# Kernel tuning notes

Measured on AMD Instinct MI355X. Metric: run time of the kernel, lower is better.

## Reference

```python
import jax, jax.numpy as jnp
import numpy as np
from jax import lax

VOCAB = 100   # chars_count
E = 32        # CHARACTER_EMBEDDING_SIZE
H = 64        # CHAR_LSTM_HIDDEN_SIZE
N_WORDS = 65536
MAX_LEN = 16


def setup_inputs() -> dict:
    key = jax.random.key(0)
    k_ch, k_len, k_emb, k_wih, k_whh, k_bih, k_bhh = jax.random.split(key, 7)
    chars = jax.random.randint(k_ch, (N_WORDS, MAX_LEN), 0, VOCAB, dtype=jnp.int32)
    lengths = jax.random.randint(k_len, (N_WORDS,), 1, MAX_LEN + 1, dtype=jnp.int32)
    s = 1.0 / np.sqrt(H)  # torch LSTM default init scale
    emb = jax.random.normal(k_emb, (VOCAB, E), dtype=jnp.float32)
    W_ih = jax.random.uniform(k_wih, (4 * H, E), minval=-s, maxval=s, dtype=jnp.float32)
    W_hh = jax.random.uniform(k_whh, (4 * H, H), minval=-s, maxval=s, dtype=jnp.float32)
    b_ih = jax.random.uniform(k_bih, (4 * H,), minval=-s, maxval=s, dtype=jnp.float32)
    b_hh = jax.random.uniform(k_bhh, (4 * H,), minval=-s, maxval=s, dtype=jnp.float32)
    return {"emb": emb, "W_ih": W_ih, "W_hh": W_hh, "b_ih": b_ih, "b_hh": b_hh,
            "chars": chars, "lengths": lengths}


def _char_lstm(emb, W_ih, W_hh, b_ih, b_hh, chars, lengths):
    N, L = chars.shape
    h0 = jnp.zeros((N, H), dtype=emb.dtype)
    c0 = jnp.zeros((N, H), dtype=emb.dtype)

    def step(carry, inp):
        h, c = carry
        ch_t, t = inp  # ch_t: [N] char ids at timestep t
        x = emb[ch_t]  # [N, E]
        gates = x @ W_ih.T + b_ih + h @ W_hh.T + b_hh  # [N, 4H]
        i_g, f_g, g_g, o_g = jnp.split(gates, 4, axis=-1)  # torch order i,f,g,o
        i_g = jax.nn.sigmoid(i_g)
        f_g = jax.nn.sigmoid(f_g)
        g_g = jnp.tanh(g_g)
        o_g = jax.nn.sigmoid(o_g)
        c_new = f_g * c + i_g * g_g
        h_new = o_g * jnp.tanh(c_new)
        active = (t < lengths)[:, None]  # freeze state past word end -> out[-1]
        h = jnp.where(active, h_new, h)
        c = jnp.where(active, c_new, c)
        return (h, c), None

    (h_final, _), _ = lax.scan(step, (h0, c0), (chars.T, jnp.arange(L)))
    return h_final  # [N, H] = last valid hidden per word


def reference(emb, W_ih, W_hh, b_ih, b_hh, chars, lengths):
    return _char_lstm(emb, W_ih, W_hh, b_ih, b_hh, chars, lengths)
```

## Files before the change

kernel.cpp:

```cpp
#include <hip/hip_runtime.h>
#include <hip/hip_bf16.h>


#define VOCAB 100
#define E     32
#define NW    65536
#define MAXL  16
#define NGRP  4096

typedef __bf16 bf16x8 __attribute__((ext_vector_type(8)));
typedef float  f32x4  __attribute__((ext_vector_type(4)));
typedef unsigned short ushort_t;
typedef unsigned int uint_t;

#define LOG2E    1.4426950408889634f
#define TWOLOG2E 2.8853900817779268f

__device__ __forceinline__ ushort_t f2bf(float x) {
    union { __hip_bfloat16 b; ushort_t u; } cv;
    cv.b = __float2bfloat16(x);
    return cv.u;
}
__device__ __forceinline__ float exp2_hw(float x) { return __builtin_amdgcn_exp2f(x); }
__device__ __forceinline__ float rcp_hw(float x)  { return __builtin_amdgcn_rcpf(x); }

__global__ void prep_fused(const float* __restrict__ emb, const float* __restrict__ Wih,
                           const float* __restrict__ Whh, const float* __restrict__ bih,
                           const float* __restrict__ bhh, const int* __restrict__ lengths,
                           float* __restrict__ xtab, ushort_t* __restrict__ Wb,
                           int* __restrict__ bh) {
    int bid = blockIdx.x;
    if (bid < VOCAB) {
        int ch = bid, g = threadIdx.x, q = g >> 6;
        float scl = (q == 2) ? TWOLOG2E : -LOG2E;
        float acc = bih[g] + bhh[g];
        const float* er = emb + ch * E;
        const float* wr = Wih + g * E;
        #pragma unroll
        for (int e = 0; e < E; ++e) acc = fmaf(er[e], wr[e], acc);
        xtab[ch * 256 + g] = acc * scl;
    } else if (bid < VOCAB + 64) {
        int i = (bid - VOCAB) * 256 + threadIdx.x;
        int q = i >> 12;
        float scl = (q == 2) ? TWOLOG2E : -LOG2E;
        Wb[i] = f2bf(Whh[i] * scl);
    } else {
        int blk = bid - (VOCAB + 64);
        __shared__ int h[16];
        if (threadIdx.x < 16) h[threadIdx.x] = 0;
        __syncthreads();
        atomicAdd(&h[lengths[blk * 256 + threadIdx.x] - 1], 1);
        __syncthreads();
        if (threadIdx.x < 16) bh[blk * 16 + threadIdx.x] = h[threadIdx.x];
    }
}

__global__ void k_bases(const int* __restrict__ bh, int* __restrict__ bases) {
    __shared__ int chunk[16][16], chunkpre[16][16], tot[16], gb[16];
    int t = threadIdx.x, b = t & 15, cs = t >> 4;
    int s = 0;
    #pragma unroll
    for (int i = 0; i < 16; ++i) s += bh[(cs * 16 + i) * 16 + b];
    chunk[cs][b] = s;
    __syncthreads();
    if (t < 16) {
        int a = 0;
        for (int c2 = 0; c2 < 16; ++c2) { chunkpre[c2][b] = a; a += chunk[c2][b]; }
        tot[b] = a;
    }
    __syncthreads();
    if (t == 0) { int a = 0; for (int i = 0; i < 16; ++i) { gb[i] = a; a += tot[i]; } }
    __syncthreads();
    int base = gb[b] + chunkpre[cs][b];
    for (int i = 0; i < 16; ++i) {
        bases[(cs * 16 + i) * 16 + b] = base;
        base += bh[(cs * 16 + i) * 16 + b];
    }
}

__global__ void k_scatter(const int* __restrict__ lengths, const int* __restrict__ bases,
                          int* __restrict__ perm) {
    __shared__ int h[16];
    if (threadIdx.x < 16) h[threadIdx.x] = 0;
    __syncthreads();
    int w = blockIdx.x * 256 + threadIdx.x;
    int b = lengths[w] - 1;
    int r = atomicAdd(&h[b], 1);
    perm[bases[blockIdx.x * 16 + b] + r] = w;
}

__global__ __launch_bounds__(256, 2) void lstm_main(
    const ushort_t* __restrict__ Wb, const float* __restrict__ xtab,
    const int* __restrict__ chars, const int* __restrict__ lengths,
    const int* __restrict__ perm, float* __restrict__ out)
{
    __shared__ __align__(16) char Hlds_all[4][2048];
    char* Hbase = Hlds_all[threadIdx.x >> 6];

    const int lane = threadIdx.x & 63;
    const int w  = lane & 15;
    const int lq = lane >> 4;
    const int widx = threadIdx.x >> 6;
    const int cls  = (widx << 2) | (blockIdx.x & 3);
    const int grp  = (cls << 8) | (blockIdx.x >> 2);

    bf16x8 a[16][2];
    #pragma unroll
    for (int m = 0; m < 16; ++m)
        #pragma unroll
        for (int kh = 0; kh < 2; ++kh)
            a[m][kh] = *reinterpret_cast<const bf16x8*>(Wb + ((m * 16 + w) * 64 + kh * 32 + lq * 8));

    const int sw = (w & 7) << 4;
    const int base_w = w * 128;
    int wr_off[4], rd_off[2];
    #pragma unroll
    for (int b = 0; b < 4; ++b) wr_off[b] = base_w + ((b * 32 + lq * 8) ^ sw);
    #pragma unroll
    for (int kh = 0; kh < 2; ++kh) rd_off[kh] = base_w + ((kh * 64 + lq * 16) ^ sw);

    const int wid = perm[grp * 16 + w];
    const int len = lengths[wid];
    int ml = len;
    ml = max(ml, __shfl_xor(ml, 1));
    ml = max(ml, __shfl_xor(ml, 2));
    ml = max(ml, __shfl_xor(ml, 4));
    ml = max(ml, __shfl_xor(ml, 8));
    const int maxl = __builtin_amdgcn_readfirstlane(ml);
    const int* chp = chars + wid * MAXL;

    float hreg[4][4], creg[4][4];
    #pragma unroll
    for (int b = 0; b < 4; ++b)
        #pragma unroll
        for (int r = 0; r < 4; ++r) { hreg[b][r] = 0.f; creg[b][r] = 0.f; }

    int ch = chp[0];
    const float* xrow = xtab + ch * 256;
    f32x4 xtb[2][4];
    #pragma unroll
    for (int q = 0; q < 4; ++q)
        xtb[0][q] = *reinterpret_cast<const f32x4*>(xrow + (q * 4 + 0) * 16 + lq * 4);

    #pragma unroll 1
    for (int t = 0; t < maxl; ++t) {
        const int tn = (t + 1 < maxl) ? t + 1 : t;
        const int ch_nxt = chp[tn];
        const float* xrow_n = xtab + ch_nxt * 256;

        bf16x8 B0, B1;
        if (t > 0) {
            asm volatile("s_waitcnt lgkmcnt(0)" ::: "memory");
            B0 = *reinterpret_cast<const bf16x8*>(Hbase + rd_off[0]);
            B1 = *reinterpret_cast<const bf16x8*>(Hbase + rd_off[1]);
        }
        const bool act = (t < len);

        #pragma unroll
        for (int b = 0; b < 4; ++b) {
            if (b < 3) {
                #pragma unroll
                for (int q = 0; q < 4; ++q)
                    xtb[(b + 1) & 1][q] = *reinterpret_cast<const f32x4*>(xrow + (q * 4 + b + 1) * 16 + lq * 4);
            } else {
                #pragma unroll
                for (int q = 0; q < 4; ++q)
                    xtb[0][q] = *reinterpret_cast<const f32x4*>(xrow_n + q * 64 + lq * 4);
            }
            f32x4 d[4];
            #pragma unroll
            for (int q = 0; q < 4; ++q) d[q] = xtb[b & 1][q];
            if (t > 0) {
                #pragma unroll
                for (int q = 0; q < 4; ++q) {
                    d[q] = __builtin_amdgcn_mfma_f32_16x16x32_bf16(a[q * 4 + b][0], B0, d[q], 0, 0, 0);
                    d[q] = __builtin_amdgcn_mfma_f32_16x16x32_bf16(a[q * 4 + b][1], B1, d[q], 0, 0, 0);
                }
            }
            #pragma unroll
            for (int r = 0; r < 4; ++r) {
                float ig = rcp_hw(1.f + exp2_hw(d[0][r]));
                float fg = rcp_hw(1.f + exp2_hw(d[1][r]));
                float gg = fmaf(-2.f, rcp_hw(1.f + exp2_hw(d[2][r])), 1.f);
                float og = rcp_hw(1.f + exp2_hw(d[3][r]));
                float cn = fmaf(fg, creg[b][r], ig * gg);
                float tc = fmaf(-2.f, rcp_hw(1.f + exp2_hw(cn * TWOLOG2E)), 1.f);
                float hn = og * tc;
                creg[b][r] = act ? cn : creg[b][r];
                hreg[b][r] = act ? hn : hreg[b][r];
            }
            uint_t lo = (uint_t)f2bf(hreg[b][0]) | ((uint_t)f2bf(hreg[b][1]) << 16);
            uint_t hi = (uint_t)f2bf(hreg[b][2]) | ((uint_t)f2bf(hreg[b][3]) << 16);
            *reinterpret_cast<uint2*>(Hbase + wr_off[b]) = make_uint2(lo, hi);
        }
        ch = ch_nxt;
        xrow = xrow_n;
    }

    #pragma unroll
    for (int b = 0; b < 4; ++b) {
        f32x4 o;
        #pragma unroll
        for (int r = 0; r < 4; ++r) o[r] = hreg[b][r];
        *reinterpret_cast<f32x4*>(out + wid * 64 + b * 16 + lq * 4) = o;
    }
}

extern "C" void kernel_launch(void* const* d_in, const int* in_sizes, int n_in,
                              void* d_out, int out_size, void* d_ws, size_t ws_size,
                              hipStream_t stream) {
    const float* emb = (const float*)d_in[0];
    const float* Wih = (const float*)d_in[1];
    const float* Whh = (const float*)d_in[2];
    const float* bih = (const float*)d_in[3];
    const float* bhh = (const float*)d_in[4];
    const int* chars = (const int*)d_in[5];
    const int* lens  = (const int*)d_in[6];
    float* out = (float*)d_out;

    float*    xtab = (float*)d_ws;
    ushort_t* Wb   = (ushort_t*)(xtab + 25600);
    int*      bh   = (int*)(Wb + 16384);
    int*      bas  = bh + 4096;
    int*      perm = bas + 4096;

    prep_fused<<<VOCAB + 64 + 256, 256, 0, stream>>>(emb, Wih, Whh, bih, bhh, lens, xtab, Wb, bh);
    k_bases<<<1, 256, 0, stream>>>(bh, bas);
    k_scatter<<<256, 256, 0, stream>>>(lens, bas, perm);

    lstm_main<<<1024, 256, 0, stream>>>(Wb, xtab, chars, lens, perm, out);
}
```

Measured before the change: 177.8 us.

## Merge sort kernels, pair long and short groups per wave, share rcp in gates

Merges the bases and scatter kernels into a single k_sort kernel, where each block recomputes its own prefix from the shared histogram, removing one launch. The LSTM kernel now launches 512 blocks, and each wave processes two length-sorted groups: group i and group NGRP-1-i. This pairs short words with long ones to balance work across waves and reuses the weight fragments loaded into registers. The gate math folds sigmoid(i)*tanh(g) and sigmoid(o)*tanh(c) into a single reciprocal each, cutting rcp instructions at some risk of overflow in the products for extreme inputs. Each wave now runs its two groups one after the other, so fewer waves are resident to hide latency.

```diff
diff --git a/kernel.cpp b/kernel.cpp
--- a/kernel.cpp
+++ b/kernel.cpp
@@ -24,11 +24,11 @@
 __device__ __forceinline__ float exp2_hw(float x) { return __builtin_amdgcn_exp2f(x); }
 __device__ __forceinline__ float rcp_hw(float x)  { return __builtin_amdgcn_rcpf(x); }
 
-__global__ void prep_fused(const float* __restrict__ emb, const float* __restrict__ Wih,
-                           const float* __restrict__ Whh, const float* __restrict__ bih,
-                           const float* __restrict__ bhh, const int* __restrict__ lengths,
-                           float* __restrict__ xtab, ushort_t* __restrict__ Wb,
-                           int* __restrict__ bh) {
+__global__ void prep_all(const float* __restrict__ emb, const float* __restrict__ Wih,
+                         const float* __restrict__ Whh, const float* __restrict__ bih,
+                         const float* __restrict__ bhh, const int* __restrict__ lengths,
+                         float* __restrict__ xtab, ushort_t* __restrict__ Wb,
+                         int* __restrict__ bh) {
     int bid = blockIdx.x;
     if (bid < VOCAB) {
         int ch = bid, g = threadIdx.x, q = g >> 6;
@@ -55,38 +55,30 @@
     }
 }
 
-__global__ void k_bases(const int* __restrict__ bh, int* __restrict__ bases) {
-    __shared__ int chunk[16][16], chunkpre[16][16], tot[16], gb[16];
-    int t = threadIdx.x, b = t & 15, cs = t >> 4;
-    int s = 0;
-    #pragma unroll
-    for (int i = 0; i < 16; ++i) s += bh[(cs * 16 + i) * 16 + b];
-    chunk[cs][b] = s;
+__global__ void k_sort(const int* __restrict__ lengths, const int* __restrict__ bh,
+                       int* __restrict__ perm) {
+    __shared__ int lbh[4096];
+    __shared__ int pre[16], tot[16], gb[16], mybase[16], hh[16];
+    const int t = threadIdx.x, B = blockIdx.x;
+    for (int i = t; i < 4096; i += 256) lbh[i] = bh[i];
+    if (t < 16) hh[t] = 0;
     __syncthreads();
     if (t < 16) {
-        int a = 0;
-        for (int c2 = 0; c2 < 16; ++c2) { chunkpre[c2][b] = a; a += chunk[c2][b]; }
-        tot[b] = a;
+        int s = 0;
+        for (int B2 = 0; B2 < B; ++B2) s += lbh[B2 * 16 + t];
+        int tt = s;
+        for (int B2 = B; B2 < 256; ++B2) tt += lbh[B2 * 16 + t];
+        pre[t] = s; tot[t] = tt;
     }
     __syncthreads();
     if (t == 0) { int a = 0; for (int i = 0; i < 16; ++i) { gb[i] = a; a += tot[i]; } }
     __syncthreads();
-    int base = gb[b] + chunkpre[cs][b];
-    for (int i = 0; i < 16; ++i) {
-        bases[(cs * 16 + i) * 16 + b] = base;
-        base += bh[(cs * 16 + i) * 16 + b];
-    }
-}
-
-__global__ void k_scatter(const int* __restrict__ lengths, const int* __restrict__ bases,
-                          int* __restrict__ perm) {
-    __shared__ int h[16];
-    if (threadIdx.x < 16) h[threadIdx.x] = 0;
-    __syncthreads();
-    int w = blockIdx.x * 256 + threadIdx.x;
+    if (t < 16) mybase[t] = gb[t] + pre[t];
+    __syncthreads();
+    int w = B * 256 + t;
     int b = lengths[w] - 1;
-    int r = atomicAdd(&h[b], 1);
-    perm[bases[blockIdx.x * 16 + b] + r] = w;
+    int r = atomicAdd(&hh[b], 1);
+    perm[mybase[b] + r] = w;
 }
 
 __global__ __launch_bounds__(256, 2) void lstm_main(
@@ -100,9 +92,7 @@
     const int lane = threadIdx.x & 63;
     const int w  = lane & 15;
     const int lq = lane >> 4;
-    const int widx = threadIdx.x >> 6;
-    const int cls  = (widx << 2) | (blockIdx.x & 3);
-    const int grp  = (cls << 8) | (blockIdx.x >> 2);
+    const int wave = (blockIdx.x << 2) + (threadIdx.x >> 6);
 
     bf16x8 a[16][2];
     #pragma unroll
@@ -119,90 +109,98 @@
     #pragma unroll
     for (int kh = 0; kh < 2; ++kh) rd_off[kh] = base_w + ((kh * 64 + lq * 16) ^ sw);
 
-    const int wid = perm[grp * 16 + w];
-    const int len = lengths[wid];
-    int ml = len;
-    ml = max(ml, __shfl_xor(ml, 1));
-    ml = max(ml, __shfl_xor(ml, 2));
-    ml = max(ml, __shfl_xor(ml, 4));
-    ml = max(ml, __shfl_xor(ml, 8));
-    const int maxl = __builtin_amdgcn_readfirstlane(ml);
-    const int* chp = chars + wid * MAXL;
-
-    float hreg[4][4], creg[4][4];
-    #pragma unroll
-    for (int b = 0; b < 4; ++b)
-        #pragma unroll
-        for (int r = 0; r < 4; ++r) { hreg[b][r] = 0.f; creg[b][r] = 0.f; }
-
-    int ch = chp[0];
-    const float* xrow = xtab + ch * 256;
-    f32x4 xtb[2][4];
-    #pragma unroll
-    for (int q = 0; q < 4; ++q)
-        xtb[0][q] = *reinterpret_cast<const f32x4*>(xrow + (q * 4 + 0) * 16 + lq * 4);
-
     #pragma unroll 1
-    for (int t = 0; t < maxl; ++t) {
-        const int tn = (t + 1 < maxl) ? t + 1 : t;
-        const int ch_nxt = chp[tn];
-        const float* xrow_n = xtab + ch_nxt * 256;
-
-        bf16x8 B0, B1;
-        if (t > 0) {
-            asm volatile("s_waitcnt lgkmcnt(0)" ::: "memory");
-            B0 = *reinterpret_cast<const bf16x8*>(Hbase + rd_off[0]);
-            B1 = *reinterpret_cast<const bf16x8*>(Hbase + rd_off[1]);
+    for (int gi = 0; gi < 2; ++gi) {
+        const int grp = gi ? (NGRP - 1 - wave) : wave;
+        const int wid = perm[grp * 16 + w];
+        const int len = lengths[wid];
+        int ml = len;
+        ml = max(ml, __shfl_xor(ml, 1));
+        ml = max(ml, __shfl_xor(ml, 2));
+        ml = max(ml, __shfl_xor(ml, 4));
+        ml = max(ml, __shfl_xor(ml, 8));
+        const int maxl = __builtin_amdgcn_readfirstlane(ml);
+        const int* chp = chars + wid * MAXL;
+
+        float hreg[4][4], creg[4][4];
+        #pragma unroll
+        for (int b = 0; b < 4; ++b)
+            #pragma unroll
+            for (int r = 0; r < 4; ++r) { hreg[b][r] = 0.f; creg[b][r] = 0.f; }
+
+        int ch = chp[0];
+        const float* xrow = xtab + ch * 256;
+        f32x4 xtb[2][4];
+        #pragma unroll
+        for (int q = 0; q < 4; ++q)
+            xtb[0][q] = *reinterpret_cast<const f32x4*>(xrow + (q * 4 + 0) * 16 + lq * 4);
+
+        #pragma unroll 1
+        for (int t = 0; t < maxl; ++t) {
+            const int tn = (t + 1 < maxl) ? t + 1 : t;
+            const int ch_nxt = chp[tn];
+            const float* xrow_n = xtab + ch_nxt * 256;
+
+            bf16x8 B0, B1;
+            if (t > 0) {
+                asm volatile("s_waitcnt lgkmcnt(0)" ::: "memory");
+                B0 = *reinterpret_cast<const bf16x8*>(Hbase + rd_off[0]);
+                B1 = *reinterpret_cast<const bf16x8*>(Hbase + rd_off[1]);
+            }
+            const bool act = (t < len);
+
+            #pragma unroll
+            for (int b = 0; b < 4; ++b) {
+                if (b < 3) {
+                    #pragma unroll
+                    for (int q = 0; q < 4; ++q)
+                        xtb[(b + 1) & 1][q] = *reinterpret_cast<const f32x4*>(xrow + (q * 4 + b + 1) * 16 + lq * 4);
+                } else {
+                    #pragma unroll
+                    for (int q = 0; q < 4; ++q)
+                        xtb[0][q] = *reinterpret_cast<const f32x4*>(xrow_n + q * 64 + lq * 4);
+                }
+                f32x4 d[4];
+                #pragma unroll
+                for (int q = 0; q < 4; ++q) d[q] = xtb[b & 1][q];
+                if (t > 0) {
+                    #pragma unroll
+                    for (int q = 0; q < 4; ++q) {
+                        d[q] = __builtin_amdgcn_mfma_f32_16x16x32_bf16(a[q * 4 + b][0], B0, d[q], 0, 0, 0);
+                        d[q] = __builtin_amdgcn_mfma_f32_16x16x32_bf16(a[q * 4 + b][1], B1, d[q], 0, 0, 0);
+                    }
+                }
+                #pragma unroll
+                for (int r = 0; r < 4; ++r) {
+                    float ui = exp2_hw(d[0][r]);
+                    float uf = exp2_hw(d[1][r]);
+                    float ug = exp2_hw(d[2][r]);
+                    float uo = exp2_hw(d[3][r]);
+                    float ti = 1.f + ui, tg = 1.f + ug;
+                    float igg = (ug - 1.f) * rcp_hw(ti * tg);
+                    float fg  = rcp_hw(1.f + uf);
+                    float cn  = fmaf(fg, creg[b][r], igg);
+                    float uc  = exp2_hw(cn * TWOLOG2E);
+                    float to  = 1.f + uo, tc = 1.f + uc;
+                    float hn  = (uc - 1.f) * rcp_hw(to * tc);
+                    creg[b][r] = act ? cn : creg[b][r];
+                    hreg[b][r] = act ? hn : hreg[b][r];
+                }
+                uint_t lo = (uint_t)f2bf(hreg[b][0]) | ((uint_t)f2bf(hreg[b][1]) << 16);
+                uint_t hi = (uint_t)f2bf(hreg[b][2]) | ((uint_t)f2bf(hreg[b][3]) << 16);
+                *reinterpret_cast<uint2*>(Hbase + wr_off[b]) = make_uint2(lo, hi);
+            }
+            ch = ch_nxt;
+            xrow = xrow_n;
         }
-        const bool act = (t < len);
 
         #pragma unroll
         for (int b = 0; b < 4; ++b) {
-            if (b < 3) {
-                #pragma unroll
-                for (int q = 0; q < 4; ++q)
-                    xtb[(b + 1) & 1][q] = *reinterpret_cast<const f32x4*>(xrow + (q * 4 + b + 1) * 16 + lq * 4);
-            } else {
-                #pragma unroll
-                for (int q = 0; q < 4; ++q)
-                    xtb[0][q] = *reinterpret_cast<const f32x4*>(xrow_n + q * 64 + lq * 4);
-            }
-            f32x4 d[4];
+            f32x4 o;
             #pragma unroll
-            for (int q = 0; q < 4; ++q) d[q] = xtb[b & 1][q];
-            if (t > 0) {
-                #pragma unroll
-                for (int q = 0; q < 4; ++q) {
-                    d[q] = __builtin_amdgcn_mfma_f32_16x16x32_bf16(a[q * 4 + b][0], B0, d[q], 0, 0, 0);
-                    d[q] = __builtin_amdgcn_mfma_f32_16x16x32_bf16(a[q * 4 + b][1], B1, d[q], 0, 0, 0);
-                }
-            }
-            #pragma unroll
-            for (int r = 0; r < 4; ++r) {
-                float ig = rcp_hw(1.f + exp2_hw(d[0][r]));
-                float fg = rcp_hw(1.f + exp2_hw(d[1][r]));
-                float gg = fmaf(-2.f, rcp_hw(1.f + exp2_hw(d[2][r])), 1.f);
-                float og = rcp_hw(1.f + exp2_hw(d[3][r]));
-                float cn = fmaf(fg, creg[b][r], ig * gg);
-                float tc = fmaf(-2.f, rcp_hw(1.f + exp2_hw(cn * TWOLOG2E)), 1.f);
-                float hn = og * tc;
-                creg[b][r] = act ? cn : creg[b][r];
-                hreg[b][r] = act ? hn : hreg[b][r];
-            }
-            uint_t lo = (uint_t)f2bf(hreg[b][0]) | ((uint_t)f2bf(hreg[b][1]) << 16);
-            uint_t hi = (uint_t)f2bf(hreg[b][2]) | ((uint_t)f2bf(hreg[b][3]) << 16);
-            *reinterpret_cast<uint2*>(Hbase + wr_off[b]) = make_uint2(lo, hi);
+            for (int r = 0; r < 4; ++r) o[r] = hreg[b][r];
+            *reinterpret_cast<f32x4*>(out + wid * 64 + b * 16 + lq * 4) = o;
         }
-        ch = ch_nxt;
-        xrow = xrow_n;
-    }
-
-    #pragma unroll
-    for (int b = 0; b < 4; ++b) {
-        f32x4 o;
-        #pragma unroll
-        for (int r = 0; r < 4; ++r) o[r] = hreg[b][r];
-        *reinterpret_cast<f32x4*>(out + wid * 64 + b * 16 + lq * 4) = o;
     }
 }
 
@@ -221,12 +219,10 @@
     float*    xtab = (float*)d_ws;
     ushort_t* Wb   = (ushort_t*)(xtab + 25600);
     int*      bh   = (int*)(Wb + 16384);
-    int*      bas  = bh + 4096;
-    int*      perm = bas + 4096;
-
-    prep_fused<<<VOCAB + 64 + 256, 256, 0, stream>>>(emb, Wih, Whh, bih, bhh, lens, xtab, Wb, bh);
-    k_bases<<<1, 256, 0, stream>>>(bh, bas);
-    k_scatter<<<256, 256, 0, stream>>>(lens, bas, perm);
-
-    lstm_main<<<1024, 256, 0, stream>>>(Wb, xtab, chars, lens, perm, out);
-}
+    int*      perm = bh + 4096;
+
+    prep_all<<<VOCAB + 64 + 256, 256, 0, stream>>>(emb, Wih, Whh, bih, bhh, lens, xtab, Wb, bh);
+    k_sort<<<256, 256, 0, stream>>>(lens, bh, perm);
+
+    lstm_main<<<512, 256, 0, stream>>>(Wb, xtab, chars, lens, perm, out);
+}
```

Measured after the change: 155.5 us. 1.14x faster.
